# Kernel tuning notes

Measured on AMD Instinct MI355X. Metric: run time of the kernel, lower is better.

## Reference

```python
import jax, jax.numpy as jnp
import numpy as np

N_ATOMS = 100000
N_EDGES = 6400000
CUTOFF = 12.0
CUTOFF_SR = 2.0
CUTOFF_SQ = CUTOFF * CUTOFF
KEHALF = 7.199822675975274  # ASE kehalf, unit factors = 1


def poly6_switch(d, cutoff):
    # Poly6 smooth switch-off: 1 at d=0, 0 at d>=cutoff
    x = d / cutoff
    sw = 1.0 - 10.0 * x**3 + 15.0 * x**4 - 6.0 * x**5
    return jnp.where(d < cutoff, sw, jnp.zeros_like(sw))


def setup_inputs() -> dict:
    key = jax.random.key(0)
    k1, k2, k3, k4, k5 = jax.random.split(key, 5)
    atomic_charges = jax.random.normal(k1, (N_ATOMS,), dtype=jnp.float32) * 0.3
    atomic_dipoles = jax.random.normal(k2, (N_ATOMS,), dtype=jnp.float32) * 0.1
    # distances in (0.5, 13.5): some pairs inside short-range, some beyond cutoff
    distances = jax.random.uniform(k3, (N_EDGES,), dtype=jnp.float32) * 13.0 + 0.5
    idx_i = jax.random.randint(k4, (N_EDGES,), 0, N_ATOMS, dtype=jnp.int32)
    idx_j = jax.random.randint(k5, (N_EDGES,), 0, N_ATOMS, dtype=jnp.int32)
    return {
        "atomic_charges": atomic_charges,
        "atomic_dipoles": atomic_dipoles,
        "distances": distances,
        "idx_i": idx_i,
        "idx_j": idx_j,
    }


def reference(atomic_charges, atomic_dipoles, distances, idx_i, idx_j):
    # gather per-edge charges / dipoles
    qi = atomic_charges[idx_i]
    qj = atomic_charges[idx_j]
    di = atomic_dipoles[idx_i]
    dj = atomic_dipoles[idx_j]

    d = distances
    d_sh = jnp.sqrt(d * d + 1.0)  # shielded distance

    sw_off = poly6_switch(d, CUTOFF_SR)
    sw_on = 1.0 - sw_off

    # split_distance=True branch (cutoff != cutoff_short_range):
    # shifted-force Coulomb (charge-charge, ~1/d)
    E_ord_q = 1.0 / d + d / CUTOFF_SQ - 2.0 / CUTOFF
    E_sh_q = 1.0 / d_sh + d_sh / CUTOFF_SQ - 2.0 / CUTOFF
    E_q = KEHALF * qi * qj * (sw_off * E_sh_q + sw_on * E_ord_q)

    # dipole-dipole term (~1/d^3), same shielded/ordinary blending
    E_ord_d = 1.0 / d**3
    E_sh_d = 1.0 / d_sh**3
    E_d = KEHALF * di * dj * (sw_off * E_sh_d + sw_on * E_ord_d)

    E = E_q + E_d
    E = jnp.where(d <= CUTOFF, E, jnp.zeros_like(E))

    # scatter-sum per-edge energies to atoms
    return jax.ops.segment_sum(E, idx_i, num_segments=N_ATOMS)
```

## Files before the change

### kernel.cpp

```cpp
#include <hip/hip_runtime.h>
#include <hip/hip_bf16.h>
#include <hip/hip_fp16.h>

#define CUTOFF_C    12.0f
#define CUTOFF_SR_C 2.0f
#define CUTOFF_SQ_C 144.0f
#define KEHALF_C    7.199822675975274f

#define BLK1   1024

#define CH_DUO   17408
#define LUT_DUO  1024
#define CH_SOLO  33792
#define LUT_SOLO 2048

#define CH_REC   20000

__device__ __forceinline__ float edge_energy(float d, float qi, float qj,
                                             float di, float dj) {
    float inv_d   = __frcp_rn(d);
    float dsh     = __fsqrt_rn(fmaf(d, d, 1.0f));
    float inv_dsh = __frcp_rn(dsh);
    float x  = d * (1.0f / CUTOFF_SR_C);
    float x3 = x * x * x;
    float sw = fmaf(x3, fmaf(x, fmaf(x, -6.0f, 15.0f), -10.0f), 1.0f);
    float sw_off = (d < CUTOFF_SR_C) ? sw : 0.0f;
    float Eoq = inv_d   + fmaf(d,   (1.0f / CUTOFF_SQ_C), -(2.0f / CUTOFF_C));
    float Esq = inv_dsh + fmaf(dsh, (1.0f / CUTOFF_SQ_C), -(2.0f / CUTOFF_C));
    float Eq  = (KEHALF_C * qi * qj) * fmaf(sw_off, Esq - Eoq, Eoq);
    float Eod = inv_d * inv_d * inv_d;
    float Esd = inv_dsh * inv_dsh * inv_dsh;
    float Ed  = (KEHALF_C * di * dj) * fmaf(sw_off, Esd - Eod, Eod);
    return Eq + Ed;
}

__device__ __forceinline__ float2 fg_exact(float d) {
    float inv_d   = 1.0f / d;
    float dsh     = sqrtf(fmaf(d, d, 1.0f));
    float inv_dsh = 1.0f / dsh;
    float x  = d * (1.0f / CUTOFF_SR_C);
    float x3 = x * x * x;
    float sw = fmaf(x3, fmaf(x, fmaf(x, -6.0f, 15.0f), -10.0f), 1.0f);
    float sw_off = (d < CUTOFF_SR_C) ? sw : 0.0f;
    float Foq = inv_d   + fmaf(d,   (1.0f / CUTOFF_SQ_C), -(2.0f / CUTOFF_C));
    float Fsq = inv_dsh + fmaf(dsh, (1.0f / CUTOFF_SQ_C), -(2.0f / CUTOFF_C));
    float F   = fmaf(sw_off, Fsq - Foq, Foq);
    float God = inv_d * inv_d * inv_d;
    float Gsd = inv_dsh * inv_dsh * inv_dsh;
    float G   = fmaf(sw_off, Gsd - God, God);
    return make_float2(KEHALF_C * F, KEHALF_C * G);
}

__device__ __forceinline__ __half2 vw_make_exact(float d, __half2 hqdj) {
    float2 qdj = __half22float2(hqdj);
    float2 fg  = fg_exact(d);
    return __floats2half2_rn(qdj.x * fg.x, qdj.y * fg.y);
}

__device__ __forceinline__ unsigned h2bits(__half2 h) {
    union { __half2 h; unsigned u; } c; c.h = h; return c.u;
}
__device__ __forceinline__ __half2 bits2h(unsigned u) {
    union { unsigned u; __half2 h; } c; c.u = u; return c.h;
}
template <typename T>
__device__ __forceinline__ auto atom_add_h2(T* p, T v, int)
    -> decltype(atomicAdd(p, v), void()) {
    atomicAdd(p, v);
}
template <typename T>
__device__ __forceinline__ void atom_add_h2(T* p, T v, long) {
    unsigned* u = (unsigned*)p;
    unsigned old = *u, assumed;
    do {
        assumed = old;
        __half2 sum = __hadd2(bits2h(assumed), v);
        old = atomicCAS(u, assumed, h2bits(sum));
    } while (old != assumed);
}

__device__ __forceinline__ unsigned vw_bits(float d, __half2 hq) {
    float inv_d   = __builtin_amdgcn_rcpf(d);
    float dsh2    = fmaf(d, d, 1.0f);
    float inv_dsh = __builtin_amdgcn_rsqf(dsh2);
    float dsh     = dsh2 * inv_dsh;
    float x  = d * (1.0f / CUTOFF_SR_C);
    float x3 = x * x * x;
    float sw = fmaf(x3, fmaf(x, fmaf(x, -6.0f, 15.0f), -10.0f), 1.0f);
    float sw_off = (d < CUTOFF_SR_C) ? sw : 0.0f;
    float Foq = inv_d   + fmaf(d,   (1.0f / CUTOFF_SQ_C), -(2.0f / CUTOFF_C));
    float Fsq = inv_dsh + fmaf(dsh, (1.0f / CUTOFF_SQ_C), -(2.0f / CUTOFF_C));
    float F   = fmaf(sw_off, Fsq - Foq, Foq);
    float God = inv_d * inv_d * inv_d;
    float Gsd = inv_dsh * inv_dsh * inv_dsh;
    float G   = fmaf(sw_off, Gsd - God, God);
    float2 q2 = __half22float2(hq);
    __half2 vw = __floats2half2_rn((KEHALF_C * q2.x) * F, (KEHALF_C * q2.y) * G);
    return h2bits(vw);
}

__global__ __launch_bounds__(256) void pc_pack_qd_h(
    const float* __restrict__ q,
    const float* __restrict__ dip,
    __half2*     __restrict__ qd,
    int n_atoms)
{
    int a = blockIdx.x * 256 + threadIdx.x;
    if (a < n_atoms) qd[a] = __floats2half2_rn(q[a], dip[a]);
}

__global__ __launch_bounds__(256) void pc_edge_vw(
    const float*   __restrict__ dist,
    const int*     __restrict__ idx_j,
    const __half2* __restrict__ qd,
    uint4*         __restrict__ vwo,
    unsigned*      __restrict__ vws,
    int n_edges, int n4, int third)
{
    const int t = blockIdx.x * 256 + (int)threadIdx.x;
    const int4*   j4p = (const int4*)idx_j;
    const float4* d4p = (const float4*)dist;

    if (t < third) {
        const int  ga = t;
        const int  gb = t + third;
        const int  gc = t + 2 * third;
        const bool vb = gb < n4;
        const bool vc = gc < n4;
        const int  gbs = vb ? gb : ga;
        const int  gcs = vc ? gc : ga;

        int4   ja = j4p[ga];
        int4   jb = j4p[gbs];
        int4   jc = j4p[gcs];
        float4 da = d4p[ga];
        float4 db = d4p[gbs];
        float4 dc = d4p[gcs];

        __half2 qa0 = qd[ja.x], qa1 = qd[ja.y], qa2 = qd[ja.z], qa3 = qd[ja.w];
        __half2 qb0 = qd[jb.x], qb1 = qd[jb.y], qb2 = qd[jb.z], qb3 = qd[jb.w];
        __half2 qc0 = qd[jc.x], qc1 = qd[jc.y], qc2 = qd[jc.z], qc3 = qd[jc.w];

        unsigned wa0 = vw_bits(da.x, qa0);
        unsigned wa1 = vw_bits(da.y, qa1);
        unsigned wa2 = vw_bits(da.z, qa2);
        unsigned wa3 = vw_bits(da.w, qa3);
        unsigned wb0 = vw_bits(db.x, qb0);
        unsigned wb1 = vw_bits(db.y, qb1);
        unsigned wb2 = vw_bits(db.z, qb2);
        unsigned wb3 = vw_bits(db.w, qb3);
        unsigned wc0 = vw_bits(dc.x, qc0);
        unsigned wc1 = vw_bits(dc.y, qc1);
        unsigned wc2 = vw_bits(dc.z, qc2);
        unsigned wc3 = vw_bits(dc.w, qc3);

        wa0 = (da.x <= CUTOFF_C) ? wa0 : 0u;
        wa1 = (da.y <= CUTOFF_C) ? wa1 : 0u;
        wa2 = (da.z <= CUTOFF_C) ? wa2 : 0u;
        wa3 = (da.w <= CUTOFF_C) ? wa3 : 0u;
        wb0 = (db.x <= CUTOFF_C) ? wb0 : 0u;
        wb1 = (db.y <= CUTOFF_C) ? wb1 : 0u;
        wb2 = (db.z <= CUTOFF_C) ? wb2 : 0u;
        wb3 = (db.w <= CUTOFF_C) ? wb3 : 0u;
        wc0 = (dc.x <= CUTOFF_C) ? wc0 : 0u;
        wc1 = (dc.y <= CUTOFF_C) ? wc1 : 0u;
        wc2 = (dc.z <= CUTOFF_C) ? wc2 : 0u;
        wc3 = (dc.w <= CUTOFF_C) ? wc3 : 0u;

        vwo[ga] = make_uint4(wa0, wa1, wa2, wa3);
        if (vb) vwo[gb] = make_uint4(wb0, wb1, wb2, wb3);
        if (vc) vwo[gc] = make_uint4(wc0, wc1, wc2, wc3);
    }

    const int tl = n_edges & 3;
    if (blockIdx.x == 0 && (int)threadIdx.x < tl) {
        int e = (n4 << 2) + (int)threadIdx.x;
        float d = dist[e];
        unsigned w = vw_bits(d, qd[idx_j[e]]);
        vws[e] = (d <= CUTOFF_C) ? w : 0u;
    }
}

template <int CH, int BLK>
__global__ __launch_bounds__(BLK) void pc_scatter_vw(
    const int*      __restrict__ idx_i,
    const unsigned* __restrict__ vw,
    __half2*        __restrict__ partial,
    int n_edges, int n4, int S, int gps, int n_atoms)
{
    extern __shared__ char smem[];
    __half2* acc2 = (__half2*)smem;

    const int s = blockIdx.x % S;
    const int c = blockIdx.x / S;
    const unsigned base = (unsigned)(c * CH);
    const int lim = min(CH, n_atoms - (int)base);

    const __half2 hzero = __floats2half2_rn(0.0f, 0.0f);
    for (int i = threadIdx.x; i < CH; i += BLK) acc2[i] = hzero;
    __syncthreads();

    const int4*  i4p = (const int4*)idx_i;
    const uint4* v4p = (const uint4*)vw;
    const int g0 = s * gps;
    const int g1 = min(g0 + gps, n4);
    for (int g = g0 + (int)threadIdx.x; g < g1; g += 2 * BLK) {
        const int  gB   = g + BLK;
        const bool hasB = gB < g1;
        const int  gBs  = hasB ? gB : g;

        int4  iA = i4p[g];
        int4  iB = i4p[gBs];
        uint4 vA = v4p[g];
        uint4 vB = v4p[gBs];

        unsigned a0 = (unsigned)iA.x - base;
        unsigned a1 = (unsigned)iA.y - base;
        unsigned a2 = (unsigned)iA.z - base;
        unsigned a3 = (unsigned)iA.w - base;
        if (a0 < (unsigned)CH) atom_add_h2(&acc2[a0], bits2h(vA.x), 0);
        if (a1 < (unsigned)CH) atom_add_h2(&acc2[a1], bits2h(vA.y), 0);
        if (a2 < (unsigned)CH) atom_add_h2(&acc2[a2], bits2h(vA.z), 0);
        if (a3 < (unsigned)CH) atom_add_h2(&acc2[a3], bits2h(vA.w), 0);
        if (hasB) {
            unsigned b0 = (unsigned)iB.x - base;
            unsigned b1 = (unsigned)iB.y - base;
            unsigned b2 = (unsigned)iB.z - base;
            unsigned b3 = (unsigned)iB.w - base;
            if (b0 < (unsigned)CH) atom_add_h2(&acc2[b0], bits2h(vB.x), 0);
            if (b1 < (unsigned)CH) atom_add_h2(&acc2[b1], bits2h(vB.y), 0);
            if (b2 < (unsigned)CH) atom_add_h2(&acc2[b2], bits2h(vB.z), 0);
            if (b3 < (unsigned)CH) atom_add_h2(&acc2[b3], bits2h(vB.w), 0);
        }
    }

    if (s == S - 1) {
        for (int e = (n4 << 2) + (int)threadIdx.x; e < n_edges; e += BLK) {
            unsigned lc = (unsigned)idx_i[e] - base;
            if (lc < (unsigned)CH) atom_add_h2(&acc2[lc], bits2h(vw[e]), 0);
        }
    }

    __syncthreads();
    __half2* row = partial + (size_t)s * n_atoms + (int)base;
    for (int i = threadIdx.x; i < lim; i += BLK) row[i] = acc2[i];
}

template <int CH, int LUTN, int BLK>
__global__ __launch_bounds__(BLK) void pc_scatter_lut(
    const float*   __restrict__ dist,
    const int*     __restrict__ idx_i,
    const int*     __restrict__ idx_j,
    const __half2* __restrict__ qd,
    __half2*       __restrict__ partial,
    int n_edges, int n4, int S, int gps, int n_atoms, int nch)
{
    extern __shared__ char smem[];
    __half2* acc2 = (__half2*)smem;
    float2*  lut  = (float2*)(smem + (size_t)CH * sizeof(__half2));

    const int s    = blockIdx.x % S;
    const int c    = blockIdx.x / S;
    const int base = c * CH;
    const int lim  = min(CH, n_atoms - base);

    const __half2 hzero = __floats2half2_rn(0.0f, 0.0f);
    for (int i = threadIdx.x; i < CH; i += BLK) acc2[i] = hzero;

    const float hstep = CUTOFF_C / (float)LUTN;
    for (int k = threadIdx.x; k <= LUTN; k += BLK) {
        float d = fmaxf((float)k * hstep, 0.25f * hstep);
        lut[k] = fg_exact(d);
    }
    __syncthreads();

    const int g0 = s * gps;
    const int g1 = min(g0 + gps, n4);
    const int4*   idxi4 = (const int4*)idx_i;
    const int4*   idxj4 = (const int4*)idx_j;
    const float4* dist4 = (const float4*)dist;
    const float   dscale = (float)LUTN / CUTOFF_C;

    for (int g = g0 + (int)threadIdx.x; g < g1; g += BLK) {
        int4   i4 = idxi4[g];
        int4   j4 = idxj4[g];
        float4 d4 = dist4[g];

        int      ii[4] = { i4.x, i4.y, i4.z, i4.w };
        int      jj[4] = { j4.x, j4.y, j4.z, j4.w };
        float    dd[4] = { d4.x, d4.y, d4.z, d4.w };
        unsigned lc[4];
        bool     vl[4];
        __half2  qh[4];

        #pragma unroll
        for (int k = 0; k < 4; ++k) {
            lc[k] = (unsigned)(ii[k] - base);
            vl[k] = (lc[k] < (unsigned)CH) && (dd[k] <= CUTOFF_C);
        }
        #pragma unroll
        for (int k = 0; k < 4; ++k)
            qh[k] = vl[k] ? qd[jj[k]] : hzero;

        #pragma unroll
        for (int k = 0; k < 4; ++k) {
            if (vl[k]) {
                float t  = dd[k] * dscale;
                int   kk = min((int)t, LUTN - 1);
                float fr = t - (float)kk;
                float2 l0 = lut[kk];
                float2 l1 = lut[kk + 1];
                float F = fmaf(fr, l1.x - l0.x, l0.x);
                float G = fmaf(fr, l1.y - l0.y, l0.y);
                float2 qdj = __half22float2(qh[k]);
                __half2 vw = __floats2half2_rn(qdj.x * F, qdj.y * G);
                atom_add_h2(&acc2[lc[k]], vw, 0);
            }
        }
    }

    if (s == S - 1) {
        for (int e = (n4 << 2) + (int)threadIdx.x; e < n_edges; e += BLK) {
            int i = idx_i[e];
            float d = dist[e];
            unsigned local = (unsigned)(i - base);
            if (local < (unsigned)CH && d <= CUTOFF_C) {
                __half2 vw = vw_make_exact(d, qd[idx_j[e]]);
                atom_add_h2(&acc2[local], vw, 0);
            }
        }
    }

    __syncthreads();
    __half2* row = partial + (size_t)s * n_atoms + base;
    for (int i = threadIdx.x; i < lim; i += BLK) row[i] = acc2[i];
}

__global__ __launch_bounds__(256) void pc_reduce_vw(
    const __half2* __restrict__ partial,
    const float*   __restrict__ q,
    const float*   __restrict__ dip,
    float*         __restrict__ out,
    int n_atoms, int S)
{
    __shared__ float2 sh[256];
    int a0   = blockIdx.x * 64;
    int lane = threadIdx.x & 63;
    int w    = threadIdx.x >> 6;
    int a    = a0 + lane;

    float sv = 0.0f, sw = 0.0f;
    if (a < n_atoms) {
        int per = S >> 2;
        const __half2* p = partial + a;
        int s = w * per, send = s + per;
        for (; s < send; ++s) {
            float2 t = __half22float2(p[(size_t)s * n_atoms]);
            sv += t.x; sw += t.y;
        }
    }
    sh[threadIdx.x] = make_float2(sv, sw);
    __syncthreads();
    if (w == 0 && a < n_atoms) {
        float2 t0 = sh[lane],       t1 = sh[64 + lane];
        float2 t2 = sh[128 + lane], t3 = sh[192 + lane];
        float fv = (t0.x + t1.x) + (t2.x + t3.x);
        float fw = (t0.y + t1.y) + (t2.y + t3.y);
        out[a] = fmaf(q[a], fv, dip[a] * fw);
    }
}

__global__ __launch_bounds__(256) void pc_dipole_edges_atomic(
    const float* __restrict__ q,
    const float* __restrict__ dip,
    const float* __restrict__ dist,
    const int*   __restrict__ idx_i,
    const int*   __restrict__ idx_j,
    float*       __restrict__ out,
    int n_edges)
{
    int t = blockIdx.x * blockDim.x + threadIdx.x;
    const int stride = gridDim.x * blockDim.x;
    for (int e = t; e < n_edges; e += stride) {
        float d = dist[e];
        if (d > CUTOFF_C) continue;
        int i = idx_i[e], j = idx_j[e];
        atomicAdd(&out[i], edge_energy(d, q[i], q[j], dip[i], dip[j]));
    }
}

static int probe_blocks(const void* f, int blk, size_t lds) {
    hipError_t e1 = hipFuncSetAttribute(
        f, hipFuncAttributeMaxDynamicSharedMemorySize, (int)lds);
    int nb = 0;
    hipError_t e2 = hipOccupancyMaxActiveBlocksPerMultiprocessor(&nb, f, blk, lds);
    if (e1 != hipSuccess || e2 != hipSuccess) return 0;
    return nb;
}

extern "C" void kernel_launch(void* const* d_in, const int* in_sizes, int n_in,
                              void* d_out, int out_size, void* d_ws, size_t ws_size,
                              hipStream_t stream) {
    const float* q     = (const float*)d_in[0];
    const float* dip   = (const float*)d_in[1];
    const float* dist  = (const float*)d_in[2];
    const int*   idx_i = (const int*)d_in[3];
    const int*   idx_j = (const int*)d_in[4];
    float*       out   = (float*)d_out;

    int n_edges = in_sizes[2];
    int n_atoms = out_size;
    int n4      = n_edges >> 2;

    size_t qd_b    = ((size_t)n_atoms * sizeof(__half2) + 255) & ~(size_t)255;
    size_t vw_b    = (((size_t)n_edges * 4) + 255) & ~(size_t)255;
    size_t lds_rec = (size_t)CH_REC * sizeof(__half2);

    int nb_rec = probe_blocks((const void*)&pc_scatter_vw<CH_REC, BLK1>,
                              BLK1, lds_rec);

    int S_new = 0, nch_new = 0;
    if (nb_rec >= 2 && n_atoms > 0 && n4 > 0 && ws_size > qd_b + vw_b) {
        nch_new = (n_atoms + CH_REC - 1) / CH_REC;
        int cap = 512;
        S_new = (cap / nch_new) & ~7;
        size_t avail = ws_size - qd_b - vw_b;
        int S_fit = (int)(avail / ((size_t)n_atoms * sizeof(__half2))) & ~7;
        if (S_fit < S_new) S_new = S_fit;
    }

    if (S_new >= 8) {
        __half2*  qd      = (__half2*)d_ws;
        unsigned* vw      = (unsigned*)((char*)d_ws + qd_b);
        __half2*  partial = (__half2*)((char*)d_ws + qd_b + vw_b);
        int       gps     = (n4 + S_new - 1) / S_new;
        int       third   = (n4 + 2) / 3;
        int       gridA   = (third + 255) / 256;
        if (gridA < 1) gridA = 1;

        pc_pack_qd_h<<<(n_atoms + 255) / 256, 256, 0, stream>>>(q, dip, qd,
                                                                n_atoms);
        pc_edge_vw<<<gridA, 256, 0, stream>>>(dist, idx_j, qd,
                                              (uint4*)vw, vw,
                                              n_edges, n4, third);
        pc_scatter_vw<CH_REC, BLK1>
            <<<S_new * nch_new, BLK1, lds_rec, stream>>>(
                idx_i, vw, partial, n_edges, n4, S_new, gps, n_atoms);
        pc_reduce_vw<<<(n_atoms + 63) / 64, 256, 0, stream>>>(
            partial, q, dip, out, n_atoms, S_new);
        return;
    }

    size_t lds_duo  = (size_t)CH_DUO  * sizeof(__half2)
                    + (size_t)(LUT_DUO  + 1) * sizeof(float2);
    size_t lds_solo = (size_t)CH_SOLO * sizeof(__half2)
                    + (size_t)(LUT_SOLO + 1) * sizeof(float2);

    int nb_duo = probe_blocks((const void*)&pc_scatter_lut<CH_DUO, LUT_DUO, BLK1>,
                              BLK1, lds_duo);
    int nb_solo = probe_blocks((const void*)&pc_scatter_lut<CH_SOLO, LUT_SOLO, BLK1>,
                               BLK1, lds_solo);

    bool use_duo = (nb_duo >= 2);
    int  CH, nch, S, cap;
    size_t lds;
    if (use_duo) {
        CH  = CH_DUO;  lds = lds_duo;
        nch = (n_atoms + CH - 1) / CH;
        cap = 512;
    } else {
        CH  = CH_SOLO; lds = lds_solo;
        nch = (n_atoms + CH - 1) / CH;
        cap = 256;
    }
    S = (cap / nch) & ~7;
    if (S < 8) S = 8;

    size_t avail = (ws_size > qd_b) ? ws_size - qd_b : 0;
    int S_fit = (int)(avail / ((size_t)n_atoms * sizeof(__half2)));
    if (S_fit < S) S = S_fit & ~7;

    bool ok = (use_duo || nb_solo >= 1) && S >= 8 && n_atoms > 0;

    if (ok) {
        __half2* qd      = (__half2*)d_ws;
        __half2* partial = (__half2*)((char*)d_ws + qd_b);
        int      gps     = (n4 + S - 1) / S;

        pc_pack_qd_h<<<(n_atoms + 255) / 256, 256, 0, stream>>>(q, dip, qd,
                                                                n_atoms);
        if (use_duo)
            pc_scatter_lut<CH_DUO, LUT_DUO, BLK1>
                <<<S * nch, BLK1, lds, stream>>>(
                    dist, idx_i, idx_j, qd, partial, n_edges, n4, S, gps,
                    n_atoms, nch);
        else
            pc_scatter_lut<CH_SOLO, LUT_SOLO, BLK1>
                <<<S * nch, BLK1, lds, stream>>>(
                    dist, idx_i, idx_j, qd, partial, n_edges, n4, S, gps,
                    n_atoms, nch);
        pc_reduce_vw<<<(n_atoms + 63) / 64, 256, 0, stream>>>(
            partial, q, dip, out, n_atoms, S);
    } else {
        hipMemsetAsync(out, 0, (size_t)n_atoms * sizeof(float), stream);
        int grid = (n_edges + 255) / 256;
        pc_dipole_edges_atomic<<<grid, 256, 0, stream>>>(
            q, dip, dist, idx_i, idx_j, out, n_edges);
    }
}
```

Measured before the change: 162.5 us.

## Stage atom charge/dipole table in LDS chunks for edge gather kernel

```diff
diff --git a/kernel.cpp b/kernel.cpp
--- a/kernel.cpp
+++ b/kernel.cpp
@@ -15,6 +15,8 @@
 #define LUT_SOLO 2048
 
 #define CH_REC   20000
+
+#define AJ_CH  33336
 
 __device__ __forceinline__ float edge_energy(float d, float qi, float qj,
                                              float di, float dj) {
@@ -79,7 +81,7 @@
     } while (old != assumed);
 }
 
-__device__ __forceinline__ unsigned vw_bits(float d, __half2 hq) {
+__device__ __forceinline__ unsigned vw_bits(float d, unsigned hqbits) {
     float inv_d   = __builtin_amdgcn_rcpf(d);
     float dsh2    = fmaf(d, d, 1.0f);
     float inv_dsh = __builtin_amdgcn_rsqf(dsh2);
@@ -94,7 +96,7 @@
     float God = inv_d * inv_d * inv_d;
     float Gsd = inv_dsh * inv_dsh * inv_dsh;
     float G   = fmaf(sw_off, Gsd - God, God);
-    float2 q2 = __half22float2(hq);
+    float2 q2 = __half22float2(bits2h(hqbits));
     __half2 vw = __floats2half2_rn((KEHALF_C * q2.x) * F, (KEHALF_C * q2.y) * G);
     return h2bits(vw);
 }
@@ -109,75 +111,119 @@
     if (a < n_atoms) qd[a] = __floats2half2_rn(q[a], dip[a]);
 }
 
-__global__ __launch_bounds__(256) void pc_edge_vw(
+__global__ __launch_bounds__(BLK1) void pc_edge_jlds(
     const float*   __restrict__ dist,
     const int*     __restrict__ idx_j,
     const __half2* __restrict__ qd,
     uint4*         __restrict__ vwo,
     unsigned*      __restrict__ vws,
-    int n_edges, int n4, int third)
+    int n_edges, int n4, int third, int n_atoms, int njc)
 {
-    const int t = blockIdx.x * 256 + (int)threadIdx.x;
+    extern __shared__ unsigned lds_qd[];
+    const int tid = (int)threadIdx.x;
+    const int t   = blockIdx.x * BLK1 + tid;
     const int4*   j4p = (const int4*)idx_j;
     const float4* d4p = (const float4*)dist;
-
-    if (t < third) {
-        const int  ga = t;
-        const int  gb = t + third;
-        const int  gc = t + 2 * third;
-        const bool vb = gb < n4;
-        const bool vc = gc < n4;
-        const int  gbs = vb ? gb : ga;
-        const int  gcs = vc ? gc : ga;
-
-        int4   ja = j4p[ga];
-        int4   jb = j4p[gbs];
-        int4   jc = j4p[gcs];
-        float4 da = d4p[ga];
-        float4 db = d4p[gbs];
-        float4 dc = d4p[gcs];
-
-        __half2 qa0 = qd[ja.x], qa1 = qd[ja.y], qa2 = qd[ja.z], qa3 = qd[ja.w];
-        __half2 qb0 = qd[jb.x], qb1 = qd[jb.y], qb2 = qd[jb.z], qb3 = qd[jb.w];
-        __half2 qc0 = qd[jc.x], qc1 = qd[jc.y], qc2 = qd[jc.z], qc3 = qd[jc.w];
-
-        unsigned wa0 = vw_bits(da.x, qa0);
-        unsigned wa1 = vw_bits(da.y, qa1);
-        unsigned wa2 = vw_bits(da.z, qa2);
-        unsigned wa3 = vw_bits(da.w, qa3);
-        unsigned wb0 = vw_bits(db.x, qb0);
-        unsigned wb1 = vw_bits(db.y, qb1);
-        unsigned wb2 = vw_bits(db.z, qb2);
-        unsigned wb3 = vw_bits(db.w, qb3);
-        unsigned wc0 = vw_bits(dc.x, qc0);
-        unsigned wc1 = vw_bits(dc.y, qc1);
-        unsigned wc2 = vw_bits(dc.z, qc2);
-        unsigned wc3 = vw_bits(dc.w, qc3);
-
-        wa0 = (da.x <= CUTOFF_C) ? wa0 : 0u;
-        wa1 = (da.y <= CUTOFF_C) ? wa1 : 0u;
-        wa2 = (da.z <= CUTOFF_C) ? wa2 : 0u;
-        wa3 = (da.w <= CUTOFF_C) ? wa3 : 0u;
-        wb0 = (db.x <= CUTOFF_C) ? wb0 : 0u;
-        wb1 = (db.y <= CUTOFF_C) ? wb1 : 0u;
-        wb2 = (db.z <= CUTOFF_C) ? wb2 : 0u;
-        wb3 = (db.w <= CUTOFF_C) ? wb3 : 0u;
-        wc0 = (dc.x <= CUTOFF_C) ? wc0 : 0u;
-        wc1 = (dc.y <= CUTOFF_C) ? wc1 : 0u;
-        wc2 = (dc.z <= CUTOFF_C) ? wc2 : 0u;
-        wc3 = (dc.w <= CUTOFF_C) ? wc3 : 0u;
-
-        vwo[ga] = make_uint4(wa0, wa1, wa2, wa3);
-        if (vb) vwo[gb] = make_uint4(wb0, wb1, wb2, wb3);
-        if (vc) vwo[gc] = make_uint4(wc0, wc1, wc2, wc3);
+    const unsigned* qdu = (const unsigned*)qd;
+
+    const bool active = t < third;
+    int  ga = 0, gb = 0, gc = 0;
+    bool vb = false, vc = false;
+    int4   ja = make_int4(0, 0, 0, 0), jb = ja, jc = ja;
+    float4 da = make_float4(0.f, 0.f, 0.f, 0.f), db = da, dc = da;
+
+    if (active) {
+        ga = t;
+        gb = t + third;
+        gc = t + 2 * third;
+        vb = gb < n4;
+        vc = gc < n4;
+        const int gbs = vb ? gb : ga;
+        const int gcs = vc ? gc : ga;
+        ja = j4p[ga];  jb = j4p[gbs];  jc = j4p[gcs];
+        da = d4p[ga];  db = d4p[gbs];  dc = d4p[gcs];
     }
 
     const int tl = n_edges & 3;
-    if (blockIdx.x == 0 && (int)threadIdx.x < tl) {
-        int e = (n4 << 2) + (int)threadIdx.x;
-        float d = dist[e];
-        unsigned w = vw_bits(d, qd[idx_j[e]]);
-        vws[e] = (d <= CUTOFF_C) ? w : 0u;
+    const bool tact = (blockIdx.x == 0) && (tid < tl);
+    int   jt = 0; float dt = 0.f;
+    if (tact) {
+        int e = (n4 << 2) + tid;
+        jt = idx_j[e];
+        dt = dist[e];
+    }
+
+    unsigned j12[12] = {
+        (unsigned)ja.x, (unsigned)ja.y, (unsigned)ja.z, (unsigned)ja.w,
+        (unsigned)jb.x, (unsigned)jb.y, (unsigned)jb.z, (unsigned)jb.w,
+        (unsigned)jc.x, (unsigned)jc.y, (unsigned)jc.z, (unsigned)jc.w };
+    unsigned qh[12] = { 0u,0u,0u,0u, 0u,0u,0u,0u, 0u,0u,0u,0u };
+    unsigned qt = 0u;
+
+    for (int c = 0; c < njc; ++c) {
+        const unsigned base = (unsigned)c * (unsigned)AJ_CH;
+        const int lim  = min(AJ_CH, n_atoms - (int)base);
+        const int lim4 = lim >> 2;
+
+        __syncthreads();
+        {
+            const uint4* src4 = (const uint4*)(qdu + base);
+            uint4* dst4 = (uint4*)lds_qd;
+            for (int i = tid; i < lim4; i += BLK1) dst4[i] = src4[i];
+            for (int i = (lim4 << 2) + tid; i < lim; i += BLK1)
+                lds_qd[i] = qdu[base + i];
+        }
+        __syncthreads();
+
+        if (active) {
+            #pragma unroll
+            for (int k = 0; k < 12; ++k) {
+                unsigned lj = j12[k] - base;
+                if (lj < (unsigned)lim) qh[k] = lds_qd[lj];
+            }
+        }
+        if (tact) {
+            unsigned lj = (unsigned)jt - base;
+            if (lj < (unsigned)lim) qt = lds_qd[lj];
+        }
+    }
+
+    if (active) {
+        unsigned w0  = vw_bits(da.x, qh[0]);
+        unsigned w1  = vw_bits(da.y, qh[1]);
+        unsigned w2  = vw_bits(da.z, qh[2]);
+        unsigned w3  = vw_bits(da.w, qh[3]);
+        unsigned w4  = vw_bits(db.x, qh[4]);
+        unsigned w5  = vw_bits(db.y, qh[5]);
+        unsigned w6  = vw_bits(db.z, qh[6]);
+        unsigned w7  = vw_bits(db.w, qh[7]);
+        unsigned w8  = vw_bits(dc.x, qh[8]);
+        unsigned w9  = vw_bits(dc.y, qh[9]);
+        unsigned w10 = vw_bits(dc.z, qh[10]);
+        unsigned w11 = vw_bits(dc.w, qh[11]);
+
+        w0  = (da.x <= CUTOFF_C) ? w0  : 0u;
+        w1  = (da.y <= CUTOFF_C) ? w1  : 0u;
+        w2  = (da.z <= CUTOFF_C) ? w2  : 0u;
+        w3  = (da.w <= CUTOFF_C) ? w3  : 0u;
+        w4  = (db.x <= CUTOFF_C) ? w4  : 0u;
+        w5  = (db.y <= CUTOFF_C) ? w5  : 0u;
+        w6  = (db.z <= CUTOFF_C) ? w6  : 0u;
+        w7  = (db.w <= CUTOFF_C) ? w7  : 0u;
+        w8  = (dc.x <= CUTOFF_C) ? w8  : 0u;
+        w9  = (dc.y <= CUTOFF_C) ? w9  : 0u;
+        w10 = (dc.z <= CUTOFF_C) ? w10 : 0u;
+        w11 = (dc.w <= CUTOFF_C) ? w11 : 0u;
+
+        vwo[ga] = make_uint4(w0, w1, w2, w3);
+        if (vb) vwo[gb] = make_uint4(w4, w5, w6, w7);
+        if (vc) vwo[gc] = make_uint4(w8, w9, w10, w11);
+    }
+
+    if (tact) {
+        int e = (n4 << 2) + tid;
+        unsigned w = vw_bits(dt, qt);
+        vws[e] = (dt <= CUTOFF_C) ? w : 0u;
     }
 }
 
@@ -412,15 +458,18 @@
     int n_atoms = out_size;
     int n4      = n_edges >> 2;
 
-    size_t qd_b    = ((size_t)n_atoms * sizeof(__half2) + 255) & ~(size_t)255;
-    size_t vw_b    = (((size_t)n_edges * 4) + 255) & ~(size_t)255;
-    size_t lds_rec = (size_t)CH_REC * sizeof(__half2);
-
-    int nb_rec = probe_blocks((const void*)&pc_scatter_vw<CH_REC, BLK1>,
-                              BLK1, lds_rec);
+    size_t qd_b     = ((size_t)n_atoms * sizeof(__half2) + 255) & ~(size_t)255;
+    size_t vw_b     = (((size_t)n_edges * 4) + 255) & ~(size_t)255;
+    size_t lds_rec  = (size_t)CH_REC * sizeof(__half2);
+    size_t lds_edge = (size_t)AJ_CH * 4;
+
+    int nb_rec  = probe_blocks((const void*)&pc_scatter_vw<CH_REC, BLK1>,
+                               BLK1, lds_rec);
+    int nb_edge = probe_blocks((const void*)&pc_edge_jlds, BLK1, lds_edge);
 
     int S_new = 0, nch_new = 0;
-    if (nb_rec >= 2 && n_atoms > 0 && n4 > 0 && ws_size > qd_b + vw_b) {
+    if (nb_rec >= 2 && nb_edge >= 1 && n_atoms > 0 && n4 > 0 &&
+        ws_size > qd_b + vw_b) {
         nch_new = (n_atoms + CH_REC - 1) / CH_REC;
         int cap = 512;
         S_new = (cap / nch_new) & ~7;
@@ -435,14 +484,14 @@
         __half2*  partial = (__half2*)((char*)d_ws + qd_b + vw_b);
         int       gps     = (n4 + S_new - 1) / S_new;
         int       third   = (n4 + 2) / 3;
-        int       gridA   = (third + 255) / 256;
+        int       gridA   = (third + BLK1 - 1) / BLK1;
+        int       njc     = (n_atoms + AJ_CH - 1) / AJ_CH;
         if (gridA < 1) gridA = 1;
 
         pc_pack_qd_h<<<(n_atoms + 255) / 256, 256, 0, stream>>>(q, dip, qd,
                                                                 n_atoms);
-        pc_edge_vw<<<gridA, 256, 0, stream>>>(dist, idx_j, qd,
-                                              (uint4*)vw, vw,
-                                              n_edges, n4, third);
+        pc_edge_jlds<<<gridA, BLK1, lds_edge, stream>>>(
+            dist, idx_j, qd, (uint4*)vw, vw, n_edges, n4, third, n_atoms, njc);
         pc_scatter_vw<CH_REC, BLK1>
             <<<S_new * nch_new, BLK1, lds_rec, stream>>>(
                 idx_i, vw, partial, n_edges, n4, S_new, gps, n_atoms);
```

Measured after the change: 164.3 us. No clear change (+1.1%).
